# Optimization experiments

Hardware: AMD Instinct MI355X
Metric: run time of the kernel (lower is better)

Reference implementation:

```python
import jax, jax.numpy as jnp
import numpy as np

B, T, D = 2, 2048, 1024
H, G, K = 16, 4, 64          # num_heads, num_kv_heads, head_dim
R = H // G                   # GQA repeat factor
F = 4096                     # mlp_dim
EPS = 1e-6


def rms_norm(x, scale, eps=EPS):
    var = jnp.mean(x.astype(jnp.float32) ** 2, axis=-1, keepdims=True)
    normed = x * jax.lax.rsqrt(var + eps)
    return (scale * normed).astype(x.dtype)


def apply_rope(x_BTHK, sin_BTK, cos_BTK):
    half = x_BTHK.shape[-1] // 2
    x1, x2 = x_BTHK[..., :half], x_BTHK[..., half:]
    s = sin_BTK[:, :, None, :]
    c = cos_BTK[:, :, None, :]
    return jnp.concatenate([x1 * c - x2 * s, x2 * c + x1 * s], axis=-1).astype(x_BTHK.dtype)


def setup_inputs() -> dict:
    key = jax.random.key(0)
    ks = jax.random.split(key, 12)
    hidden_BTD = jax.random.normal(ks[0], (B, T, D), jnp.float32)
    # rope tables: realistic sin/cos of position*inv_freq
    inv_freq = 1.0 / (10000.0 ** (jnp.arange(K // 2, dtype=jnp.float32) / (K // 2)))
    ang = jnp.arange(T, dtype=jnp.float32)[:, None] * inv_freq[None, :]  # [T, K/2]
    sin_BTK = jnp.broadcast_to(jnp.sin(ang)[None], (B, T, K // 2))
    cos_BTK = jnp.broadcast_to(jnp.cos(ang)[None], (B, T, K // 2))
    mask = jnp.broadcast_to(jnp.tril(jnp.ones((T, T), bool))[None], (B, T, T))
    sc = 1.0 / np.sqrt(D)
    scf = 1.0 / np.sqrt(F)
    return {
        "hidden_BTD": hidden_BTD, "sin_BTK": sin_BTK, "cos_BTK": cos_BTK, "mask": mask,
        "ln1_scale": jnp.ones((D,), jnp.float32),
        "ln2_scale": jnp.ones((D,), jnp.float32),
        "qn_scale": jnp.ones((K,), jnp.float32),
        "kn_scale": jnp.ones((K,), jnp.float32),
        "q_w": jax.random.normal(ks[1], (D, H * K), jnp.float32) * sc,
        "k_w": jax.random.normal(ks[2], (D, G * K), jnp.float32) * sc,
        "v_w": jax.random.normal(ks[3], (D, G * K), jnp.float32) * sc,
        "o_w": jax.random.normal(ks[4], (H * K, D), jnp.float32) * sc,
        "gate_w": jax.random.normal(ks[5], (D, F), jnp.float32) * sc,
        "up_w": jax.random.normal(ks[6], (D, F), jnp.float32) * sc,
        "down_w": jax.random.normal(ks[7], (F, D), jnp.float32) * scf,
    }


def reference(hidden_BTD, sin_BTK, cos_BTK, mask, ln1_scale, ln2_scale,
              qn_scale, kn_scale, q_w, k_w, v_w, o_w, gate_w, up_w, down_w):
    x = rms_norm(hidden_BTD, ln1_scale)
    q = rms_norm((x @ q_w).reshape(B, T, H, K), qn_scale)
    k = rms_norm((x @ k_w).reshape(B, T, G, K), kn_scale)
    v = (x @ v_w).reshape(B, T, G, K)
    q = apply_rope(q, sin_BTK, cos_BTK)
    k = apply_rope(k, sin_BTK, cos_BTK)
    q_BTGRK = q.reshape(B, T, G, R, K)
    scale = K ** (-0.5)
    logits = jnp.einsum('BTGRK,BSGK->BTSGR', q_BTGRK, k) * scale
    neg = float(jnp.finfo(logits.dtype).min)
    logits = jnp.where(mask[:, :, :, None, None], logits, neg)
    weights = jax.nn.softmax(logits.astype(jnp.float32), axis=2).astype(logits.dtype)
    attn = jnp.einsum('BTSGR,BSGK->BTGRK', weights, v).reshape(B, T, H * K)
    hidden_BTD = hidden_BTD + attn @ o_w
    y = rms_norm(hidden_BTD, ln2_scale)
    ff = (jax.nn.silu(y @ gate_w) * (y @ up_w)) @ down_w
    return hidden_BTD + ff
```

## Files before the change

kernel.cpp:

```cpp
#include <hip/hip_runtime.h>
#include <hip/hip_bf16.h>

#define EPSF 1e-6f
constexpr int Bsz  = 2;
constexpr int Tseq = 2048;
constexpr int Dmod = 1024;
constexpr int Hh   = 16;
constexpr int Gg   = 4;
constexpr int Ff   = 4096;
constexpr int Mrows = Bsz * Tseq;

typedef __attribute__((ext_vector_type(8))) short bf16x8;
typedef __attribute__((ext_vector_type(4))) float f32x4;
typedef unsigned short u16;

__device__ inline u16 f2bf(float x) {
    union { float f; unsigned u; } v; v.f = x;
    unsigned r = v.u + 0x7fff + ((v.u >> 16) & 1);
    return (u16)(r >> 16);
}
__device__ inline float bf2f(u16 h) {
    union { unsigned u; float f; } v; v.u = ((unsigned)h) << 16; return v.f;
}

__device__ __forceinline__ void async_copy16(const u16* g, u16* l) {
    __builtin_amdgcn_global_load_lds(
        (const __attribute__((address_space(1))) void*)g,
        (__attribute__((address_space(3))) void*)l, 16, 0, 0);
}


__global__ __launch_bounds__(256) void wprep_all_kernel(
    const float* __restrict__ q_w, const float* __restrict__ k_w,
    const float* __restrict__ v_w, const float* __restrict__ o_w,
    const float* __restrict__ gate_w, const float* __restrict__ up_w,
    const float* __restrict__ down_w,
    u16* __restrict__ QKVT, u16* __restrict__ OTh, u16* __restrict__ OTl,
    u16* __restrict__ GTh, u16* __restrict__ UTh, u16* __restrict__ DTh)
{
    const int bx = blockIdx.x;
    const float* W; u16* Th; u16* Tl = nullptr;
    int N, Kd, ntile, ktile, drow;
    if (bx < 1024) {
        W = q_w; N = 1024; Kd = 1024; ntile = bx & 31; ktile = bx >> 5;
        Th = QKVT; drow = ntile * 32;
    } else if (bx < 1280) {
        const int i = bx - 1024;
        W = k_w; N = 256; Kd = 1024; ntile = i & 7; ktile = i >> 3;
        Th = QKVT; drow = 1024 + ntile * 32;
    } else if (bx < 1536) {
        const int i = bx - 1280;
        W = v_w; N = 256; Kd = 1024; ntile = i & 7; ktile = i >> 3;
        Th = QKVT; drow = 1280 + ntile * 32;
    } else if (bx < 2560) {
        const int i = bx - 1536;
        W = o_w; N = 1024; Kd = 1024; ntile = i & 31; ktile = i >> 5;
        Th = OTh; Tl = OTl; drow = ntile * 32;
    } else if (bx < 6656) {
        const int i = bx - 2560;
        W = gate_w; N = 4096; Kd = 1024; ntile = i & 127; ktile = i >> 7;
        Th = GTh; drow = ntile * 32;
    } else if (bx < 10752) {
        const int i = bx - 6656;
        W = up_w; N = 4096; Kd = 1024; ntile = i & 127; ktile = i >> 7;
        Th = UTh; drow = ntile * 32;
    } else {
        const int i = bx - 10752;
        W = down_w; N = 1024; Kd = 4096; ntile = i & 31; ktile = i >> 5;
        Th = DTh; drow = ntile * 32;
    }
    const int n0 = ntile * 32, k0 = ktile * 32;

    __shared__ float tile[32][33];
    const int r = threadIdx.x >> 3, c4 = (threadIdx.x & 7) * 4;
    const float4 v = *reinterpret_cast<const float4*>(&W[(size_t)(k0 + r) * N + n0 + c4]);
    tile[r][c4 + 0] = v.x; tile[r][c4 + 1] = v.y;
    tile[r][c4 + 2] = v.z; tile[r][c4 + 3] = v.w;
    __syncthreads();
    const int nl = threadIdx.x >> 3, kq = (threadIdx.x & 7) * 4;
    float x0 = tile[kq + 0][nl], x1 = tile[kq + 1][nl];
    float x2 = tile[kq + 2][nl], x3 = tile[kq + 3][nl];
    ushort4 h;
    h.x = f2bf(x0); h.y = f2bf(x1); h.z = f2bf(x2); h.w = f2bf(x3);
    *reinterpret_cast<ushort4*>(&Th[(size_t)(drow + nl) * Kd + k0 + kq]) = h;
    if (Tl) {
        ushort4 l;
        l.x = f2bf(x0 - bf2f(h.x)); l.y = f2bf(x1 - bf2f(h.y));
        l.z = f2bf(x2 - bf2f(h.z)); l.w = f2bf(x3 - bf2f(h.w));
        *reinterpret_cast<ushort4*>(&Tl[(size_t)(drow + nl) * Kd + k0 + kq]) = l;
    }
}

template <int LO>
__global__ __launch_bounds__(256) void rmsnorm_split_kernel(
    const float* __restrict__ x, const float* __restrict__ scale,
    u16* __restrict__ oh, u16* __restrict__ ol)
{
    const int row = blockIdx.x;
    const int tid = threadIdx.x;
    const float4 v = reinterpret_cast<const float4*>(x + (size_t)row * Dmod)[tid];
    float ss = v.x * v.x + v.y * v.y + v.z * v.z + v.w * v.w;
    #pragma unroll
    for (int off = 32; off; off >>= 1) ss += __shfl_xor(ss, off, 64);
    __shared__ float part[4];
    if ((tid & 63) == 0) part[tid >> 6] = ss;
    __syncthreads();
    const float tot = part[0] + part[1] + part[2] + part[3];
    const float rstd = rsqrtf(tot * (1.0f / Dmod) + EPSF);
    const float4 sc = reinterpret_cast<const float4*>(scale)[tid];
    float o0 = v.x * rstd * sc.x, o1 = v.y * rstd * sc.y;
    float o2 = v.z * rstd * sc.z, o3 = v.w * rstd * sc.w;
    ushort4 h;
    h.x = f2bf(o0); h.y = f2bf(o1); h.z = f2bf(o2); h.w = f2bf(o3);
    *reinterpret_cast<ushort4*>(&oh[(size_t)row * Dmod + tid * 4]) = h;
    if (LO) {
        ushort4 l;
        l.x = f2bf(o0 - bf2f(h.x)); l.y = f2bf(o1 - bf2f(h.y));
        l.z = f2bf(o2 - bf2f(h.z)); l.w = f2bf(o3 - bf2f(h.w));
        *reinterpret_cast<ushort4*>(&ol[(size_t)row * Dmod + tid * 4]) = l;
    }
}

template <int NKT, int ASPLIT, int BSPLIT, int RES>
__global__ __launch_bounds__(256, 2) void mfma_gemm_pipe(
    const u16* __restrict__ Ah, const u16* __restrict__ Al,
    const u16* __restrict__ Bh, const u16* __restrict__ Bl,
    const float* __restrict__ res, float* __restrict__ C,
    int M, int N)
{
    constexpr int Kd = NKT * 32;
    constexpr int NI = 4 + 2 * ASPLIT + 2 * BSPLIT;
    static_assert((NKT - 2) % 3 == 0, "main loop unroll-3");

    __shared__ u16 AsH[3][128 * 32];
    __shared__ u16 BsH[3][128 * 32];
    __shared__ u16 AsL[ASPLIT ? 3 : 1][128 * 32];
    __shared__ u16 BsL[BSPLIT ? 3 : 1][128 * 32];

    const int tid = threadIdx.x;
    const int lane = tid & 63, wave = tid >> 6;
    const int wm = (wave >> 1) * 64, wn = (wave & 1) * 64;
    const int m0 = blockIdx.y * 128, n0 = blockIdx.x * 128;
    const int fm = lane & 15, quad = lane >> 4;
    const int fsw = (fm >> 1) & 3;
    const int fcol = (quad ^ fsw) * 8;

    f32x4 acc[4][4];
    #pragma unroll
    for (int i = 0; i < 4; ++i)
        #pragma unroll
        for (int j = 0; j < 4; ++j) acc[i][j] = (f32x4){0.f, 0.f, 0.f, 0.f};

    const int srow = tid >> 2;
    const int schk = tid & 3;
    const int sw   = schk ^ ((srow >> 1) & 3);
    const u16* aS0 = &Ah[(size_t)(m0 + srow) * Kd + sw * 8];
    const u16* aS1 = &Ah[(size_t)(m0 + srow + 64) * Kd + sw * 8];
    const u16* bS0 = &Bh[(size_t)(n0 + srow) * Kd + sw * 8];
    const u16* bS1 = &Bh[(size_t)(n0 + srow + 64) * Kd + sw * 8];
    const u16* alS0 = ASPLIT ? &Al[(size_t)(m0 + srow) * Kd + sw * 8] : nullptr;
    const u16* alS1 = ASPLIT ? &Al[(size_t)(m0 + srow + 64) * Kd + sw * 8] : nullptr;
    const u16* blS0 = BSPLIT ? &Bl[(size_t)(n0 + srow) * Kd + sw * 8] : nullptr;
    const u16* blS1 = BSPLIT ? &Bl[(size_t)(n0 + srow + 64) * Kd + sw * 8] : nullptr;
    const int dst0 = srow * 32 + schk * 8;
    const int dst1 = dst0 + 64 * 32;

#define PSTAGE(T, BUF) do {                                                  \
        async_copy16(aS0 + (T) * 32, &AsH[BUF][dst0]);                       \
        async_copy16(aS1 + (T) * 32, &AsH[BUF][dst1]);                       \
        if (ASPLIT) {                                                        \
            async_copy16(alS0 + (T) * 32, &AsL[BUF][dst0]);                  \
            async_copy16(alS1 + (T) * 32, &AsL[BUF][dst1]);                  \
        }                                                                    \
        async_copy16(bS0 + (T) * 32, &BsH[BUF][dst0]);                       \
        async_copy16(bS1 + (T) * 32, &BsH[BUF][dst1]);                       \
        if (BSPLIT) {                                                        \
            async_copy16(blS0 + (T) * 32, &BsL[BUF][dst0]);                  \
            async_copy16(blS1 + (T) * 32, &BsL[BUF][dst1]);                  \
        }                                                                    \
    } while (0)

#define PGATE(GATE) do {                                                     \
        if ((GATE) == 1) {                                                   \
            if constexpr (NI == 4)                                           \
                asm volatile("s_waitcnt vmcnt(4)" ::: "memory");             \
            else                                                             \
                asm volatile("s_waitcnt vmcnt(8)" ::: "memory");             \
        } else if ((GATE) == 0) {                                            \
            asm volatile("s_waitcnt vmcnt(0)" ::: "memory");                 \
        }                                                                    \
    } while (0)

#define PSTEP(BC, BN, T, PF, GATE) do {                                      \
    bf16x8 ah[4], bh[4], al[4], bl[4];                                       \
    _Pragma("unroll")                                                        \
    for (int t = 0; t < 4; ++t) {                                            \
        const int ra = (wm + t * 16 + fm) * 32 + fcol;                       \
        const int rb = (wn + t * 16 + fm) * 32 + fcol;                       \
        ah[t] = *reinterpret_cast<const bf16x8*>(&AsH[BC][ra]);              \
        bh[t] = *reinterpret_cast<const bf16x8*>(&BsH[BC][rb]);              \
        if (ASPLIT) al[t] = *reinterpret_cast<const bf16x8*>(&AsL[BC][ra]);  \
        if (BSPLIT) bl[t] = *reinterpret_cast<const bf16x8*>(&BsL[BC][rb]);  \
    }                                                                        \
    if (PF) PSTAGE((T) + 2, BN);                                             \
    __builtin_amdgcn_s_barrier();                                            \
    asm volatile("s_waitcnt lgkmcnt(0)" ::: "memory");                       \
    __builtin_amdgcn_sched_barrier(0);                                       \
    __builtin_amdgcn_s_setprio(1);                                           \
    _Pragma("unroll")                                                        \
    for (int mt = 0; mt < 4; ++mt)                                           \
        _Pragma("unroll")                                                    \
        for (int nt = 0; nt < 4; ++nt) {                                     \
            acc[mt][nt] = __builtin_amdgcn_mfma_f32_16x16x32_bf16(           \
                ah[mt], bh[nt], acc[mt][nt], 0, 0, 0);                       \
            if (BSPLIT)                                                      \
                acc[mt][nt] = __builtin_amdgcn_mfma_f32_16x16x32_bf16(       \
                    ah[mt], bl[nt], acc[mt][nt], 0, 0, 0);                   \
            if (ASPLIT)                                                      \
                acc[mt][nt] = __builtin_amdgcn_mfma_f32_16x16x32_bf16(       \
                    al[mt], bh[nt], acc[mt][nt], 0, 0, 0);                   \
        }                                                                    \
    __builtin_amdgcn_s_setprio(0);                                           \
    PGATE(GATE);                                                             \
    __builtin_amdgcn_s_barrier();                                            \
} while (0)

    PSTAGE(0, 0);
    PSTAGE(1, 1);
    PGATE(1);
    __builtin_amdgcn_s_barrier();

    #pragma unroll 1
    for (int t3 = 0; t3 < NKT - 2; t3 += 3) {
        PSTEP(0, 2, t3 + 0, true, 1);
        PSTEP(1, 0, t3 + 1, true, 1);
        PSTEP(2, 1, t3 + 2, true, 1);
    }
    PSTEP(0, 2, NKT - 2, false, 0);
    PSTEP(1, 0, NKT - 1, false, -1);

#undef PSTEP
#undef PGATE
#undef PSTAGE

    const int cr = (lane >> 4) * 4, cn = lane & 15;
    #pragma unroll
    for (int mt = 0; mt < 4; ++mt)
        #pragma unroll
        for (int nt = 0; nt < 4; ++nt)
            #pragma unroll
            for (int r = 0; r < 4; ++r) {
                const int gm = m0 + wm + mt * 16 + cr + r;
                const int gn = n0 + wn + nt * 16 + cn;
                float v = acc[mt][nt][r];
                if (RES) v += res[(size_t)gm * N + gn];
                C[(size_t)gm * N + gn] = v;
            }
}

__global__ __launch_bounds__(256, 2) void qkv_fused_kernel(
    const u16* __restrict__ Ah, const u16* __restrict__ Bh,
    const float* __restrict__ qn, const float* __restrict__ kn,
    const float* __restrict__ sinp, const float* __restrict__ cosp,
    u16* __restrict__ Qbh, u16* __restrict__ Qbl,
    u16* __restrict__ Kbh, u16* __restrict__ Kbl,
    u16* __restrict__ Vth, u16* __restrict__ Vtl)
{
    constexpr int Kd = 1024;
    constexpr int NKT = 32;
    __shared__ u16 As[3][128 * 32];
    __shared__ u16 Bs[3][128 * 32];

    const int tid = threadIdx.x;
    const int lane = tid & 63, wave = tid >> 6;
    const int wm = (wave >> 1) * 64, wn = (wave & 1) * 64;
    const int m0 = blockIdx.y * 128, n0 = blockIdx.x * 128;
    const int fm = lane & 15, quad = lane >> 4;
    const int fsw = (fm >> 1) & 3;
    const int fcol = ((quad ^ fsw) * 8);

    f32x4 acc[4][4];
    #pragma unroll
    for (int i = 0; i < 4; ++i)
        #pragma unroll
        for (int j = 0; j < 4; ++j) acc[i][j] = (f32x4){0.f, 0.f, 0.f, 0.f};

    const int srow = tid >> 2;
    const int schk = tid & 3;
    const int sw   = schk ^ ((srow >> 1) & 3);
    const u16* aS0 = &Ah[(size_t)(m0 + srow) * Kd + sw * 8];
    const u16* aS1 = &Ah[(size_t)(m0 + srow + 64) * Kd + sw * 8];
    const u16* bS0 = &Bh[(size_t)(n0 + srow) * Kd + sw * 8];
    const u16* bS1 = &Bh[(size_t)(n0 + srow + 64) * Kd + sw * 8];
    const int dst0 = srow * 32 + schk * 8;
    const int dst1 = dst0 + 64 * 32;

#define QSTAGE(T, BUF) do {                                                  \
        async_copy16(aS0 + (T) * 32, &As[BUF][dst0]);                        \
        async_copy16(aS1 + (T) * 32, &As[BUF][dst1]);                        \
        async_copy16(bS0 + (T) * 32, &Bs[BUF][dst0]);                        \
        async_copy16(bS1 + (T) * 32, &Bs[BUF][dst1]);                        \
    } while (0)

#define QSTEP(BC, BN, T, PF, GATE) do {                                      \
    bf16x8 ah[4], bh[4];                                                     \
    _Pragma("unroll")                                                        \
    for (int t = 0; t < 4; ++t) {                                            \
        ah[t] = *reinterpret_cast<const bf16x8*>(                            \
            &As[BC][(wm + t * 16 + fm) * 32 + fcol]);                        \
        bh[t] = *reinterpret_cast<const bf16x8*>(                            \
            &Bs[BC][(wn + t * 16 + fm) * 32 + fcol]);                        \
    }                                                                        \
    if (PF) QSTAGE((T) + 2, BN);                                             \
    __builtin_amdgcn_s_barrier();                                            \
    asm volatile("s_waitcnt lgkmcnt(0)" ::: "memory");                       \
    __builtin_amdgcn_sched_barrier(0);                                       \
    __builtin_amdgcn_s_setprio(1);                                           \
    _Pragma("unroll")                                                        \
    for (int mt = 0; mt < 4; ++mt)                                           \
        _Pragma("unroll")                                                    \
        for (int nt = 0; nt < 4; ++nt)                                       \
            acc[mt][nt] = __builtin_amdgcn_mfma_f32_16x16x32_bf16(           \
                ah[mt], bh[nt], acc[mt][nt], 0, 0, 0);                       \
    __builtin_amdgcn_s_setprio(0);                                           \
    if ((GATE) == 1) {                                                       \
        asm volatile("s_waitcnt vmcnt(4)" ::: "memory");                     \
    } else if ((GATE) == 0) {                                                \
        asm volatile("s_waitcnt vmcnt(0)" ::: "memory");                     \
    }                                                                        \
    __builtin_amdgcn_s_barrier();                                            \
} while (0)

    QSTAGE(0, 0);
    QSTAGE(1, 1);
    asm volatile("s_waitcnt vmcnt(4)" ::: "memory");
    __builtin_amdgcn_s_barrier();

    #pragma unroll 1
    for (int t3 = 0; t3 < NKT - 2; t3 += 3) {
        QSTEP(0, 2, t3 + 0, true, 1);
        QSTEP(1, 0, t3 + 1, true, 1);
        QSTEP(2, 1, t3 + 2, true, 1);
    }
    QSTEP(0, 2, NKT - 2, false, 0);
    QSTEP(1, 0, NKT - 1, false, -1);

#undef QSTEP
#undef QSTAGE

    const int gn0 = n0 + wn;
    const int l15 = lane & 15;

    if (gn0 < 1280) {
        const bool isQ = (gn0 < 1024);
        const float* nsc = isQ ? qn : kn;
        const float osc = isQ ? 0.125f : 1.0f;
        u16* __restrict__ oh = isQ ? Qbh : Kbh;
        u16* __restrict__ ol = isQ ? Qbl : Kbl;
        const int rowstride = isQ ? 1024 : 256;
        const int colbase = isQ ? gn0 : gn0 - 1024;
        float sc[4];
        #pragma unroll
        for (int nt = 0; nt < 4; ++nt) sc[nt] = nsc[nt * 16 + l15];

        #pragma unroll
        for (int mt = 0; mt < 4; ++mt)
            #pragma unroll
            for (int r = 0; r < 4; ++r) {
                const int bt = m0 + wm + mt * 16 + quad * 4 + r;
                float v[4];
                #pragma unroll
                for (int nt = 0; nt < 4; ++nt) v[nt] = acc[mt][nt][r];
                float ss = v[0] * v[0] + v[1] * v[1] + v[2] * v[2] + v[3] * v[3];
                #pragma unroll
                for (int off = 1; off < 16; off <<= 1)
                    ss += __shfl_xor(ss, off, 16);
                const float rstd = rsqrtf(ss * (1.0f / 64.0f) + EPSF);
                float nv[4];
                #pragma unroll
                for (int nt = 0; nt < 4; ++nt) nv[nt] = v[nt] * rstd * sc[nt];
                const float s0 = sinp[bt * 32 + l15];
                const float c0 = cosp[bt * 32 + l15];
                const float s1 = sinp[bt * 32 + 16 + l15];
                const float c1 = cosp[bt * 32 + 16 + l15];
                float o[4];
                o[0] = (nv[0] * c0 - nv[2] * s0) * osc;
                o[1] = (nv[1] * c1 - nv[3] * s1) * osc;
                o[2] = (nv[2] * c0 + nv[0] * s0) * osc;
                o[3] = (nv[3] * c1 + nv[1] * s1) * osc;
                #pragma unroll
                for (int nt = 0; nt < 4; ++nt) {
                    const size_t off = (size_t)bt * rowstride + colbase + nt * 16 + l15;
                    const u16 hi = f2bf(o[nt]);
                    oh[off] = hi;
                    ol[off] = f2bf(o[nt] - bf2f(hi));
                }
            }
    } else {
        const int g = (gn0 - 1280) >> 6;
        const int b = (m0 + wm) >> 11;
        const int tb = ((m0 + wm) & 2047) + quad * 4;
        #pragma unroll
        for (int mt = 0; mt < 4; ++mt)
            #pragma unroll
            for (int nt = 0; nt < 4; ++nt) {
                const float v0 = acc[mt][nt][0], v1 = acc[mt][nt][1];
                const float v2 = acc[mt][nt][2], v3 = acc[mt][nt][3];
                ushort4 hv, lv;
                hv.x = f2bf(v0); hv.y = f2bf(v1); hv.z = f2bf(v2); hv.w = f2bf(v3);
                lv.x = f2bf(v0 - bf2f(hv.x)); lv.y = f2bf(v1 - bf2f(hv.y));
                lv.z = f2bf(v2 - bf2f(hv.z)); lv.w = f2bf(v3 - bf2f(hv.w));
                const size_t off =
                    ((size_t)((b * 4 + g) * 64 + nt * 16 + l15)) * Tseq + tb + mt * 16;
                *reinterpret_cast<ushort4*>(&Vth[off]) = hv;
                *reinterpret_cast<ushort4*>(&Vtl[off]) = lv;
            }
    }
}

#define GU_PHASE_SYNC()                                       \
    __builtin_amdgcn_s_barrier();                             \
    asm volatile("s_waitcnt lgkmcnt(0)" ::: "memory");        \
    __builtin_amdgcn_sched_barrier(0)

#define GU_MFMA16(AF, NB0)                                                       \
    _Pragma("unroll")                                                            \
    for (int mf = 0; mf < 4; ++mf) {                                             \
        accg[mf][(NB0)] = __builtin_amdgcn_mfma_f32_16x16x32_bf16(               \
            AF[mf], bgf[(NB0)], accg[mf][(NB0)], 0, 0, 0);                       \
        accu[mf][(NB0)] = __builtin_amdgcn_mfma_f32_16x16x32_bf16(               \
            AF[mf], buf2[(NB0)], accu[mf][(NB0)], 0, 0, 0);                      \
        accg[mf][(NB0) + 1] = __builtin_amdgcn_mfma_f32_16x16x32_bf16(           \
            AF[mf], bgf[(NB0) + 1], accg[mf][(NB0) + 1], 0, 0, 0);               \
        accu[mf][(NB0) + 1] = __builtin_amdgcn_mfma_f32_16x16x32_bf16(           \
            AF[mf], buf2[(NB0) + 1], accu[mf][(NB0) + 1], 0, 0, 0);              \
    }

__global__ __launch_bounds__(512, 2) void gateup8_kernel(
    const u16* __restrict__ Yh, const u16* __restrict__ Yl,
    const u16* __restrict__ Gw, const u16* __restrict__ Uw,
    u16* __restrict__ FF)
{
    constexpr int NK = 32;
    __shared__ u16 AsH[3][256 * 32];
    __shared__ u16 AsL[3][256 * 32];
    __shared__ u16 Gs[3][128 * 32];
    __shared__ u16 Us[3][128 * 32];

    const int tid  = threadIdx.x;
    const int lane = tid & 63;
    const int wave = tid >> 6;
    const int wave_m = wave >> 1;
    const int wave_n = wave & 1;

    const int wg  = blockIdx.x;
    const int xcd = wg & 7;
    const int idx = wg >> 3;
    const int ntile = xcd * 4 + (idx & 3);
    const int mtile = idx >> 2;
    const int m0 = mtile * 256, n0 = ntile * 128;

    const int fm = lane & 15, quad = lane >> 4;
    const int fsw = (fm >> 1) & 3;
    const int fcol = (quad ^ fsw) * 8;

    f32x4 accg[4][4], accu[4][4];
    #pragma unroll
    for (int i = 0; i < 4; ++i)
        #pragma unroll
        for (int j = 0; j < 4; ++j) {
            accg[i][j] = (f32x4){0.f, 0.f, 0.f, 0.f};
            accu[i][j] = (f32x4){0.f, 0.f, 0.f, 0.f};
        }

    const int srow = tid >> 2;
    const int schk = tid & 3;
    const int sw   = schk ^ ((srow >> 1) & 3);
    const u16* aSrc0 = &Yh[(size_t)(m0 + srow) * 1024 + sw * 8];
    const u16* aSrc1 = &Yh[(size_t)(m0 + srow + 128) * 1024 + sw * 8];
    const u16* lSrc0 = &Yl[(size_t)(m0 + srow) * 1024 + sw * 8];
    const u16* lSrc1 = &Yl[(size_t)(m0 + srow + 128) * 1024 + sw * 8];
    const u16* gSrc  = &Gw[(size_t)(n0 + srow) * 1024 + sw * 8];
    const u16* uSrc  = &Uw[(size_t)(n0 + srow) * 1024 + sw * 8];
    const int aDst0 = srow * 32 + schk * 8;
    const int aDst1 = aDst0 + 128 * 32;

#define STAGE_AH(T, BUF) do {                                  \
        async_copy16(aSrc0 + (T) * 32, &AsH[BUF][aDst0]);      \
        async_copy16(aSrc1 + (T) * 32, &AsH[BUF][aDst1]); } while (0)
#define STAGE_AL(T, BUF) do {                                  \
        async_copy16(lSrc0 + (T) * 32, &AsL[BUF][aDst0]);      \
        async_copy16(lSrc1 + (T) * 32, &AsL[BUF][aDst1]); } while (0)
#define STAGE_B(T, BUF) do {                                   \
        async_copy16(gSrc + (T) * 32, &Gs[BUF][aDst0]);        \
        async_copy16(uSrc + (T) * 32, &Us[BUF][aDst0]); } while (0)

    int raOff[4], rbOff[4];
    #pragma unroll
    for (int mf = 0; mf < 4; ++mf)
        raOff[mf] = (wave_m * 64 + mf * 16 + fm) * 32 + fcol;
    #pragma unroll
    for (int nf = 0; nf < 4; ++nf)
        rbOff[nf] = (wave_n * 64 + nf * 16 + fm) * 32 + fcol;

    STAGE_AH(0, 0); STAGE_AL(0, 0); STAGE_B(0, 0);
    STAGE_AH(1, 1); STAGE_AL(1, 1); STAGE_B(1, 1);
    asm volatile("s_waitcnt vmcnt(6)" ::: "memory");
    __builtin_amdgcn_s_barrier();

    int bcur = 0, bnxt = 2;
    #pragma unroll 1
    for (int t = 0; t < NK; ++t) {
        const bool pf = (t + 2 < NK);
        bf16x8 bgf[4], buf2[4];
        bf16x8 ahf[4];

        {
            #pragma unroll
            for (int nf = 0; nf < 4; ++nf) {
                bgf[nf]  = *reinterpret_cast<const bf16x8*>(&Gs[bcur][rbOff[nf]]);
                buf2[nf] = *reinterpret_cast<const bf16x8*>(&Us[bcur][rbOff[nf]]);
            }
            #pragma unroll
            for (int mf = 0; mf < 4; ++mf)
                ahf[mf] = *reinterpret_cast<const bf16x8*>(&AsH[bcur][raOff[mf]]);
            if (pf) STAGE_AH(t + 2, bnxt);
            GU_PHASE_SYNC();
            __builtin_amdgcn_s_setprio(1);
            GU_MFMA16(ahf, 0);
            __builtin_amdgcn_s_setprio(0);
            __builtin_amdgcn_s_barrier();
        }
        {
            if (pf) STAGE_AL(t + 2, bnxt);
            GU_PHASE_SYNC();
            __builtin_amdgcn_s_setprio(1);
            GU_MFMA16(ahf, 2);
            __builtin_amdgcn_s_setprio(0);
            __builtin_amdgcn_s_barrier();
        }
        bf16x8 alf[4];
        {
            #pragma unroll
            for (int mf = 0; mf < 4; ++mf)
                alf[mf] = *reinterpret_cast<const bf16x8*>(&AsL[bcur][raOff[mf]]);
            if (pf) STAGE_B(t + 2, bnxt);
            GU_PHASE_SYNC();
            __builtin_amdgcn_s_setprio(1);
            GU_MFMA16(alf, 0);
            __builtin_amdgcn_s_setprio(0);
            __builtin_amdgcn_s_barrier();
        }
        {
            GU_PHASE_SYNC();
            __builtin_amdgcn_s_setprio(1);
            GU_MFMA16(alf, 2);
            __builtin_amdgcn_s_setprio(0);
            if (t + 2 < NK) {
                asm volatile("s_waitcnt vmcnt(6)" ::: "memory");
            } else if (t + 1 < NK) {
                asm volatile("s_waitcnt vmcnt(0)" ::: "memory");
            }
            __builtin_amdgcn_s_barrier();
        }

        bcur = (bcur == 2) ? 0 : bcur + 1;
        bnxt = (bnxt == 2) ? 0 : bnxt + 1;
    }
#undef STAGE_AH
#undef STAGE_AL
#undef STAGE_B

    const int cr = quad * 4;
    #pragma unroll
    for (int mf = 0; mf < 4; ++mf)
        #pragma unroll
        for (int nf = 0; nf < 4; ++nf)
            #pragma unroll
            for (int r = 0; r < 4; ++r) {
                const int gm = m0 + wave_m * 64 + mf * 16 + cr + r;
                const int gn = n0 + wave_n * 64 + nf * 16 + fm;
                const float g = accg[mf][nf][r];
                const float ff = (g / (1.0f + __expf(-g))) * accu[mf][nf][r];
                FF[(size_t)gm * Ff + gn] = f2bf(ff);
            }
}

__global__ __launch_bounds__(256) void attn_mfma_kernel(
    const u16* __restrict__ Qh, const u16* __restrict__ Ql,
    const u16* __restrict__ Kh, const u16* __restrict__ Kl,
    const u16* __restrict__ Vth, const u16* __restrict__ Vtl,
    u16* __restrict__ AOh, u16* __restrict__ AOl)
{
    __shared__ u16 KsH[64 * 72];
    __shared__ u16 KsL[64 * 72];
    __shared__ u16 VsH[64 * 72];
    __shared__ u16 VsL[64 * 72];
    __shared__ u16 Ps[4][16 * 72];

    const int tid = threadIdx.x;
    const int wave = tid >> 6, lane = tid & 63;
    const int l15 = lane & 15, quad = lane >> 4;

    const int bg = blockIdx.x & 7;
    const int b = bg >> 2, g = bg & 3;
    const int win = 127 - (blockIdx.x >> 3);
    const int t0 = win * 16;
    const int h = g * 4 + wave;

    bf16x8 qh[2], ql[2];
    {
        const size_t qrow = (size_t)(b * Tseq + t0 + l15) * 1024 + h * 64;
        #pragma unroll
        for (int ks = 0; ks < 2; ++ks) {
            qh[ks] = *reinterpret_cast<const bf16x8*>(&Qh[qrow + ks * 32 + quad * 8]);
            ql[ks] = *reinterpret_cast<const bf16x8*>(&Ql[qrow + ks * 32 + quad * 8]);
        }
    }

    const int srow = tid >> 2;
    const int scol = (tid & 3) * 16;
    const size_t kgb = (size_t)(b * Tseq) * 256 + g * 64 + scol;
    const size_t vgb = (size_t)(bg * 64 + srow) * Tseq + scol;

    const int nit = t0 / 64 + 1;

    uint4 ck0, ck1, cl0, cl1, cv0, cv1, cw0, cw1;
    {
        const size_t ka = kgb + (size_t)srow * 256;
        ck0 = *reinterpret_cast<const uint4*>(&Kh[ka]);
        ck1 = *reinterpret_cast<const uint4*>(&Kh[ka + 8]);
        cl0 = *reinterpret_cast<const uint4*>(&Kl[ka]);
        cl1 = *reinterpret_cast<const uint4*>(&Kl[ka + 8]);
        cv0 = *reinterpret_cast<const uint4*>(&Vth[vgb]);
        cv1 = *reinterpret_cast<const uint4*>(&Vth[vgb + 8]);
        cw0 = *reinterpret_cast<const uint4*>(&Vtl[vgb]);
        cw1 = *reinterpret_cast<const uint4*>(&Vtl[vgb + 8]);
    }

    f32x4 oacc[4];
    #pragma unroll
    for (int nt = 0; nt < 4; ++nt) oacc[nt] = (f32x4){0.f, 0.f, 0.f, 0.f};
    float m_r[4], l_r[4];
    #pragma unroll
    for (int r = 0; r < 4; ++r) { m_r[r] = -1e30f; l_r[r] = 0.0f; }

    u16* psw = &Ps[wave][0];
    const int lb = srow * 72 + scol;

    for (int it = 0; it < nit; ++it) {
        const int s0 = it * 64;
        const bool diag = (it == nit - 1);

        __syncthreads();
        *reinterpret_cast<uint4*>(&KsH[lb])     = ck0;
        *reinterpret_cast<uint4*>(&KsH[lb + 8]) = ck1;
        *reinterpret_cast<uint4*>(&KsL[lb])     = cl0;
        *reinterpret_cast<uint4*>(&KsL[lb + 8]) = cl1;
        *reinterpret_cast<uint4*>(&VsH[lb])     = cv0;
        *reinterpret_cast<uint4*>(&VsH[lb + 8]) = cv1;
        *reinterpret_cast<uint4*>(&VsL[lb])     = cw0;
        *reinterpret_cast<uint4*>(&VsL[lb + 8]) = cw1;
        if (it + 1 < nit) {
            const size_t ka = kgb + (size_t)(s0 + 64 + srow) * 256;
            ck0 = *reinterpret_cast<const uint4*>(&Kh[ka]);
            ck1 = *reinterpret_cast<const uint4*>(&Kh[ka + 8]);
            cl0 = *reinterpret_cast<const uint4*>(&Kl[ka]);
            cl1 = *reinterpret_cast<const uint4*>(&Kl[ka + 8]);
            const size_t va = vgb + s0 + 64;
            cv0 = *reinterpret_cast<const uint4*>(&Vth[va]);
            cv1 = *reinterpret_cast<const uint4*>(&Vth[va + 8]);
            cw0 = *reinterpret_cast<const uint4*>(&Vtl[va]);
            cw1 = *reinterpret_cast<const uint4*>(&Vtl[va + 8]);
        }
        __syncthreads();

        f32x4 sacc[4];
        #pragma unroll
        for (int nt = 0; nt < 4; ++nt) sacc[nt] = (f32x4){0.f, 0.f, 0.f, 0.f};

        #pragma unroll
        for (int ks = 0; ks < 2; ++ks) {
            bf16x8 kfh[4], kfl[4];
            #pragma unroll
            for (int nt = 0; nt < 4; ++nt) {
                const int a = (nt * 16 + l15) * 72 + ks * 32 + quad * 8;
                kfh[nt] = *reinterpret_cast<const bf16x8*>(&KsH[a]);
                kfl[nt] = *reinterpret_cast<const bf16x8*>(&KsL[a]);
            }
            #pragma unroll
            for (int nt = 0; nt < 4; ++nt) {
                sacc[nt] = __builtin_amdgcn_mfma_f32_16x16x32_bf16(qh[ks], kfh[nt], sacc[nt], 0, 0, 0);
                sacc[nt] = __builtin_amdgcn_mfma_f32_16x16x32_bf16(ql[ks], kfh[nt], sacc[nt], 0, 0, 0);
                sacc[nt] = __builtin_amdgcn_mfma_f32_16x16x32_bf16(qh[ks], kfl[nt], sacc[nt], 0, 0, 0);
            }
        }

        if (diag) {
            #pragma unroll
            for (int nt = 0; nt < 4; ++nt) {
                const int sg = s0 + nt * 16 + l15;
                #pragma unroll
                for (int r = 0; r < 4; ++r)
                    if (sg > t0 + quad * 4 + r) sacc[nt][r] = -1e30f;
            }
        }

        #pragma unroll
        for (int r = 0; r < 4; ++r) {
            float mx = fmaxf(fmaxf(sacc[0][r], sacc[1][r]),
                             fmaxf(sacc[2][r], sacc[3][r]));
            #pragma unroll
            for (int off = 1; off < 16; off <<= 1)
                mx = fmaxf(mx, __shfl_xor(mx, off, 16));
            const float mnew = fmaxf(m_r[r], mx);
            const float alpha = __expf(m_r[r] - mnew);
            m_r[r] = mnew;

            float rs = 0.0f;
            #pragma unroll
            for (int nt = 0; nt < 4; ++nt) {
                const float p = __expf(sacc[nt][r] - mnew);
                sacc[nt][r] = p;
                rs += p;
            }
            #pragma unroll
            for (int off = 1; off < 16; off <<= 1)
                rs += __shfl_xor(rs, off, 16);
            l_r[r] = l_r[r] * alpha + rs;
            #pragma unroll
            for (int nt = 0; nt < 4; ++nt) oacc[nt][r] *= alpha;
            #pragma unroll
            for (int nt = 0; nt < 4; ++nt)
                psw[(quad * 4 + r) * 72 + nt * 16 + l15] = f2bf(sacc[nt][r]);
        }

        #pragma unroll
        for (int ks = 0; ks < 2; ++ks) {
            const bf16x8 pa = *reinterpret_cast<const bf16x8*>(
                &psw[l15 * 72 + ks * 32 + quad * 8]);
            bf16x8 vfh[4], vfl[4];
            #pragma unroll
            for (int nt = 0; nt < 4; ++nt) {
                const int a = (nt * 16 + l15) * 72 + ks * 32 + quad * 8;
                vfh[nt] = *reinterpret_cast<const bf16x8*>(&VsH[a]);
                vfl[nt] = *reinterpret_cast<const bf16x8*>(&VsL[a]);
            }
            #pragma unroll
            for (int nt = 0; nt < 4; ++nt) {
                oacc[nt] = __builtin_amdgcn_mfma_f32_16x16x32_bf16(pa, vfh[nt], oacc[nt], 0, 0, 0);
                oacc[nt] = __builtin_amdgcn_mfma_f32_16x16x32_bf16(pa, vfl[nt], oacc[nt], 0, 0, 0);
            }
        }
    }

    #pragma unroll
    for (int r = 0; r < 4; ++r) {
        const float inv = 1.0f / l_r[r];
        const size_t orow = (size_t)(b * Tseq + t0 + quad * 4 + r) * 1024 + h * 64;
        #pragma unroll
        for (int nt = 0; nt < 4; ++nt) {
            const float o = oacc[nt][r] * inv;
            const u16 hi = f2bf(o);
            AOh[orow + nt * 16 + l15] = hi;
            AOl[orow + nt * 16 + l15] = f2bf(o - bf2f(hi));
        }
    }
}

extern "C" void kernel_launch(void* const* d_in, const int* in_sizes, int n_in,
                              void* d_out, int out_size, void* d_ws,
                              size_t ws_size, hipStream_t stream)
{
    const float* hidden = (const float*)d_in[0];
    const float* sinp   = (const float*)d_in[1];
    const float* cosp   = (const float*)d_in[2];
    const float* ln1    = (const float*)d_in[4];
    const float* ln2    = (const float*)d_in[5];
    const float* qn     = (const float*)d_in[6];
    const float* kn     = (const float*)d_in[7];
    const float* q_w    = (const float*)d_in[8];
    const float* k_w    = (const float*)d_in[9];
    const float* v_w    = (const float*)d_in[10];
    const float* o_w    = (const float*)d_in[11];
    const float* gate_w = (const float*)d_in[12];
    const float* up_w   = (const float*)d_in[13];
    const float* down_w = (const float*)d_in[14];
    float* out = (float*)d_out;

    char* base = (char*)d_ws;
    u16*   OTh  = (u16*)(base);
    u16*   OTl  = (u16*)(base + 2097152);
    u16*   GTh  = (u16*)(base + 4194304);
    u16*   UTh  = (u16*)(base + 12582912);
    u16*   DTh  = (u16*)(base + 20971520);
    u16*   QKVT = (u16*)(base + 29360128);
    u16*   Xh   = (u16*)(base + 32505856);
    u16*   Qbh  = (u16*)(base + 40894464);
    u16*   Qbl  = (u16*)(base + 49283072);
    u16*   Kbh  = (u16*)(base + 57671680);
    u16*   Kbl  = (u16*)(base + 59768832);
    u16*   Vth  = (u16*)(base + 61865984);
    u16*   Vtl  = (u16*)(base + 63963136);
    u16*   AOh  = (u16*)(base + 66060288);
    u16*   AOl  = (u16*)(base + 74448896);
    u16*   FFh  = (u16*)(base + 82837504);

    float* H2 = (float*)Qbh;
    u16*   Yh = Kbh;
    u16*   Yl = AOh;

    wprep_all_kernel<<<14848, 256, 0, stream>>>(
        q_w, k_w, v_w, o_w, gate_w, up_w, down_w,
        QKVT, OTh, OTl, GTh, UTh, DTh);

    rmsnorm_split_kernel<0><<<Mrows, 256, 0, stream>>>(hidden, ln1, Xh, nullptr);

    qkv_fused_kernel<<<dim3(12, 32), 256, 0, stream>>>(
        Xh, QKVT, qn, kn, sinp, cosp, Qbh, Qbl, Kbh, Kbl, Vth, Vtl);

    attn_mfma_kernel<<<Bsz * Gg * (Tseq / 16), 256, 0, stream>>>(
        Qbh, Qbl, Kbh, Kbl, Vth, Vtl, AOh, AOl);

    mfma_gemm_pipe<32, 1, 1, 1><<<dim3(8, 32), 256, 0, stream>>>(
        AOh, AOl, OTh, OTl, hidden, H2, Mrows, Dmod);

    rmsnorm_split_kernel<1><<<Mrows, 256, 0, stream>>>(H2, ln2, Yh, Yl);

    gateup8_kernel<<<512, 512, 0, stream>>>(Yh, Yl, GTh, UTh, FFh);

    mfma_gemm_pipe<128, 0, 0, 1><<<dim3(8, 32), 256, 0, stream>>>(
        FFh, nullptr, DTh, nullptr, H2, out, Mrows, Dmod);
}
```

Baseline: 496.2 us.

## Narrow output GEMM tiles to 128x64 and reshape gate/up wave layout to 2x4

The o-projection and down-projection GEMMs become templated on the N tile width and launch with BN=64. That doubles the grid from 256 to 512 blocks, so the CUs are better filled on a device with many compute units, at the cost of more A re-reads and a lower MFMA-to-load ratio. The gate/up kernel changes its 8 waves from a 4x2 to a 2x4 arrangement, with each wave covering 128x32 instead of 64x64. A fragments are now reloaded per half-phase, which changes LDS traffic and register pressure. Wait-count gating is adjusted to match the new number of loads per stage.

```diff
diff --git a/kernel.cpp b/kernel.cpp
--- a/kernel.cpp
+++ b/kernel.cpp
@@ -121,7 +121,7 @@
     }
 }
 
-template <int NKT, int ASPLIT, int BSPLIT, int RES>
+template <int NKT, int BN, int ASPLIT, int BSPLIT, int RES>
 __global__ __launch_bounds__(256, 2) void mfma_gemm_pipe(
     const u16* __restrict__ Ah, const u16* __restrict__ Al,
     const u16* __restrict__ Bh, const u16* __restrict__ Bl,
@@ -129,27 +129,28 @@
     int M, int N)
 {
     constexpr int Kd = NKT * 32;
-    constexpr int NI = 4 + 2 * ASPLIT + 2 * BSPLIT;
+    constexpr int NT = (BN / 2) / 16;
+    constexpr int NI = 2 + 2 * ASPLIT + (BN / 64) + (BN / 64) * BSPLIT;
     static_assert((NKT - 2) % 3 == 0, "main loop unroll-3");
 
     __shared__ u16 AsH[3][128 * 32];
-    __shared__ u16 BsH[3][128 * 32];
+    __shared__ u16 BsH[3][BN * 32];
     __shared__ u16 AsL[ASPLIT ? 3 : 1][128 * 32];
-    __shared__ u16 BsL[BSPLIT ? 3 : 1][128 * 32];
+    __shared__ u16 BsL[BSPLIT ? 3 : 1][BN * 32];
 
     const int tid = threadIdx.x;
     const int lane = tid & 63, wave = tid >> 6;
-    const int wm = (wave >> 1) * 64, wn = (wave & 1) * 64;
-    const int m0 = blockIdx.y * 128, n0 = blockIdx.x * 128;
+    const int wm = (wave >> 1) * 64, wn = (wave & 1) * (BN / 2);
+    const int m0 = blockIdx.y * 128, n0 = blockIdx.x * BN;
     const int fm = lane & 15, quad = lane >> 4;
     const int fsw = (fm >> 1) & 3;
     const int fcol = (quad ^ fsw) * 8;
 
-    f32x4 acc[4][4];
+    f32x4 acc[4][NT];
     #pragma unroll
     for (int i = 0; i < 4; ++i)
         #pragma unroll
-        for (int j = 0; j < 4; ++j) acc[i][j] = (f32x4){0.f, 0.f, 0.f, 0.f};
+        for (int j = 0; j < NT; ++j) acc[i][j] = (f32x4){0.f, 0.f, 0.f, 0.f};
 
     const int srow = tid >> 2;
     const int schk = tid & 3;
@@ -157,11 +158,11 @@
     const u16* aS0 = &Ah[(size_t)(m0 + srow) * Kd + sw * 8];
     const u16* aS1 = &Ah[(size_t)(m0 + srow + 64) * Kd + sw * 8];
     const u16* bS0 = &Bh[(size_t)(n0 + srow) * Kd + sw * 8];
-    const u16* bS1 = &Bh[(size_t)(n0 + srow + 64) * Kd + sw * 8];
+    const u16* bS1 = (BN == 128) ? &Bh[(size_t)(n0 + srow + 64) * Kd + sw * 8] : nullptr;
     const u16* alS0 = ASPLIT ? &Al[(size_t)(m0 + srow) * Kd + sw * 8] : nullptr;
     const u16* alS1 = ASPLIT ? &Al[(size_t)(m0 + srow + 64) * Kd + sw * 8] : nullptr;
     const u16* blS0 = BSPLIT ? &Bl[(size_t)(n0 + srow) * Kd + sw * 8] : nullptr;
-    const u16* blS1 = BSPLIT ? &Bl[(size_t)(n0 + srow + 64) * Kd + sw * 8] : nullptr;
+    const u16* blS1 = (BSPLIT && BN == 128) ? &Bl[(size_t)(n0 + srow + 64) * Kd + sw * 8] : nullptr;
     const int dst0 = srow * 32 + schk * 8;
     const int dst1 = dst0 + 64 * 32;
 
@@ -173,17 +174,21 @@
             async_copy16(alS1 + (T) * 32, &AsL[BUF][dst1]);                  \
         }                                                                    \
         async_copy16(bS0 + (T) * 32, &BsH[BUF][dst0]);                       \
-        async_copy16(bS1 + (T) * 32, &BsH[BUF][dst1]);                       \
+        if (BN == 128) async_copy16(bS1 + (T) * 32, &BsH[BUF][dst1]);        \
         if (BSPLIT) {                                                        \
             async_copy16(blS0 + (T) * 32, &BsL[BUF][dst0]);                  \
-            async_copy16(blS1 + (T) * 32, &BsL[BUF][dst1]);                  \
+            if (BN == 128) async_copy16(blS1 + (T) * 32, &BsL[BUF][dst1]);   \
         }                                                                    \
     } while (0)
 
 #define PGATE(GATE) do {                                                     \
         if ((GATE) == 1) {                                                   \
-            if constexpr (NI == 4)                                           \
+            if constexpr (NI == 3)                                           \
+                asm volatile("s_waitcnt vmcnt(3)" ::: "memory");             \
+            else if constexpr (NI == 4)                                      \
                 asm volatile("s_waitcnt vmcnt(4)" ::: "memory");             \
+            else if constexpr (NI == 6)                                      \
+                asm volatile("s_waitcnt vmcnt(6)" ::: "memory");             \
             else                                                             \
                 asm volatile("s_waitcnt vmcnt(8)" ::: "memory");             \
         } else if ((GATE) == 0) {                                            \
@@ -191,18 +196,21 @@
         }                                                                    \
     } while (0)
 
-#define PSTEP(BC, BN, T, PF, GATE) do {                                      \
-    bf16x8 ah[4], bh[4], al[4], bl[4];                                       \
+#define PSTEP(BC, BN_, T, PF, GATE) do {                                     \
+    bf16x8 ah[4], bh[NT], al[4], bl[NT];                                     \
     _Pragma("unroll")                                                        \
     for (int t = 0; t < 4; ++t) {                                            \
         const int ra = (wm + t * 16 + fm) * 32 + fcol;                       \
+        ah[t] = *reinterpret_cast<const bf16x8*>(&AsH[BC][ra]);              \
+        if (ASPLIT) al[t] = *reinterpret_cast<const bf16x8*>(&AsL[BC][ra]);  \
+    }                                                                        \
+    _Pragma("unroll")                                                        \
+    for (int t = 0; t < NT; ++t) {                                           \
         const int rb = (wn + t * 16 + fm) * 32 + fcol;                       \
-        ah[t] = *reinterpret_cast<const bf16x8*>(&AsH[BC][ra]);              \
         bh[t] = *reinterpret_cast<const bf16x8*>(&BsH[BC][rb]);              \
-        if (ASPLIT) al[t] = *reinterpret_cast<const bf16x8*>(&AsL[BC][ra]);  \
         if (BSPLIT) bl[t] = *reinterpret_cast<const bf16x8*>(&BsL[BC][rb]);  \
     }                                                                        \
-    if (PF) PSTAGE((T) + 2, BN);                                             \
+    if (PF) PSTAGE((T) + 2, BN_);                                            \
     __builtin_amdgcn_s_barrier();                                            \
     asm volatile("s_waitcnt lgkmcnt(0)" ::: "memory");                       \
     __builtin_amdgcn_sched_barrier(0);                                       \
@@ -210,7 +218,7 @@
     _Pragma("unroll")                                                        \
     for (int mt = 0; mt < 4; ++mt)                                           \
         _Pragma("unroll")                                                    \
-        for (int nt = 0; nt < 4; ++nt) {                                     \
+        for (int nt = 0; nt < NT; ++nt) {                                    \
             acc[mt][nt] = __builtin_amdgcn_mfma_f32_16x16x32_bf16(           \
                 ah[mt], bh[nt], acc[mt][nt], 0, 0, 0);                       \
             if (BSPLIT)                                                      \
@@ -247,7 +255,7 @@
     #pragma unroll
     for (int mt = 0; mt < 4; ++mt)
         #pragma unroll
-        for (int nt = 0; nt < 4; ++nt)
+        for (int nt = 0; nt < NT; ++nt)
             #pragma unroll
             for (int r = 0; r < 4; ++r) {
                 const int gm = m0 + wm + mt * 16 + cr + r;
@@ -423,17 +431,17 @@
     asm volatile("s_waitcnt lgkmcnt(0)" ::: "memory");        \
     __builtin_amdgcn_sched_barrier(0)
 
-#define GU_MFMA16(AF, NB0)                                                       \
+#define GU_MFMA4(MBASE, AF)                                                      \
     _Pragma("unroll")                                                            \
     for (int mf = 0; mf < 4; ++mf) {                                             \
-        accg[mf][(NB0)] = __builtin_amdgcn_mfma_f32_16x16x32_bf16(               \
-            AF[mf], bgf[(NB0)], accg[mf][(NB0)], 0, 0, 0);                       \
-        accu[mf][(NB0)] = __builtin_amdgcn_mfma_f32_16x16x32_bf16(               \
-            AF[mf], buf2[(NB0)], accu[mf][(NB0)], 0, 0, 0);                      \
-        accg[mf][(NB0) + 1] = __builtin_amdgcn_mfma_f32_16x16x32_bf16(           \
-            AF[mf], bgf[(NB0) + 1], accg[mf][(NB0) + 1], 0, 0, 0);               \
-        accu[mf][(NB0) + 1] = __builtin_amdgcn_mfma_f32_16x16x32_bf16(           \
-            AF[mf], buf2[(NB0) + 1], accu[mf][(NB0) + 1], 0, 0, 0);              \
+        accg[(MBASE) + mf][0] = __builtin_amdgcn_mfma_f32_16x16x32_bf16(         \
+            AF[mf], bgf[0], accg[(MBASE) + mf][0], 0, 0, 0);                     \
+        accu[(MBASE) + mf][0] = __builtin_amdgcn_mfma_f32_16x16x32_bf16(         \
+            AF[mf], buf2[0], accu[(MBASE) + mf][0], 0, 0, 0);                    \
+        accg[(MBASE) + mf][1] = __builtin_amdgcn_mfma_f32_16x16x32_bf16(         \
+            AF[mf], bgf[1], accg[(MBASE) + mf][1], 0, 0, 0);                     \
+        accu[(MBASE) + mf][1] = __builtin_amdgcn_mfma_f32_16x16x32_bf16(         \
+            AF[mf], buf2[1], accu[(MBASE) + mf][1], 0, 0, 0);                    \
     }
 
 __global__ __launch_bounds__(512, 2) void gateup8_kernel(
@@ -450,8 +458,8 @@
     const int tid  = threadIdx.x;
     const int lane = tid & 63;
     const int wave = tid >> 6;
-    const int wave_m = wave >> 1;
-    const int wave_n = wave & 1;
+    const int wave_m = wave >> 2;
+    const int wave_n = wave & 3;
 
     const int wg  = blockIdx.x;
     const int xcd = wg & 7;
@@ -464,11 +472,11 @@
     const int fsw = (fm >> 1) & 3;
     const int fcol = (quad ^ fsw) * 8;
 
-    f32x4 accg[4][4], accu[4][4];
-    #pragma unroll
-    for (int i = 0; i < 4; ++i)
-        #pragma unroll
-        for (int j = 0; j < 4; ++j) {
+    f32x4 accg[8][2], accu[8][2];
+    #pragma unroll
+    for (int i = 0; i < 8; ++i)
+        #pragma unroll
+        for (int j = 0; j < 2; ++j) {
             accg[i][j] = (f32x4){0.f, 0.f, 0.f, 0.f};
             accu[i][j] = (f32x4){0.f, 0.f, 0.f, 0.f};
         }
@@ -495,13 +503,13 @@
         async_copy16(gSrc + (T) * 32, &Gs[BUF][aDst0]);        \
         async_copy16(uSrc + (T) * 32, &Us[BUF][aDst0]); } while (0)
 
-    int raOff[4], rbOff[4];
-    #pragma unroll
-    for (int mf = 0; mf < 4; ++mf)
-        raOff[mf] = (wave_m * 64 + mf * 16 + fm) * 32 + fcol;
-    #pragma unroll
-    for (int nf = 0; nf < 4; ++nf)
-        rbOff[nf] = (wave_n * 64 + nf * 16 + fm) * 32 + fcol;
+    int raOff[8], rbOff[2];
+    #pragma unroll
+    for (int mf = 0; mf < 8; ++mf)
+        raOff[mf] = (wave_m * 128 + mf * 16 + fm) * 32 + fcol;
+    #pragma unroll
+    for (int nf = 0; nf < 2; ++nf)
+        rbOff[nf] = (wave_n * 32 + nf * 16 + fm) * 32 + fcol;
 
     STAGE_AH(0, 0); STAGE_AL(0, 0); STAGE_B(0, 0);
     STAGE_AH(1, 1); STAGE_AL(1, 1); STAGE_B(1, 1);
@@ -512,49 +520,57 @@
     #pragma unroll 1
     for (int t = 0; t < NK; ++t) {
         const bool pf = (t + 2 < NK);
-        bf16x8 bgf[4], buf2[4];
-        bf16x8 ahf[4];
+        bf16x8 bgf[2], buf2[2];
 
         {
             #pragma unroll
-            for (int nf = 0; nf < 4; ++nf) {
+            for (int nf = 0; nf < 2; ++nf) {
                 bgf[nf]  = *reinterpret_cast<const bf16x8*>(&Gs[bcur][rbOff[nf]]);
                 buf2[nf] = *reinterpret_cast<const bf16x8*>(&Us[bcur][rbOff[nf]]);
             }
+            bf16x8 af[4];
             #pragma unroll
             for (int mf = 0; mf < 4; ++mf)
-                ahf[mf] = *reinterpret_cast<const bf16x8*>(&AsH[bcur][raOff[mf]]);
+                af[mf] = *reinterpret_cast<const bf16x8*>(&AsH[bcur][raOff[mf]]);
             if (pf) STAGE_AH(t + 2, bnxt);
             GU_PHASE_SYNC();
             __builtin_amdgcn_s_setprio(1);
-            GU_MFMA16(ahf, 0);
+            GU_MFMA4(0, af);
             __builtin_amdgcn_s_setprio(0);
             __builtin_amdgcn_s_barrier();
         }
         {
+            bf16x8 af[4];
+            #pragma unroll
+            for (int mf = 0; mf < 4; ++mf)
+                af[mf] = *reinterpret_cast<const bf16x8*>(&AsH[bcur][raOff[mf + 4]]);
             if (pf) STAGE_AL(t + 2, bnxt);
             GU_PHASE_SYNC();
             __builtin_amdgcn_s_setprio(1);
-            GU_MFMA16(ahf, 2);
+            GU_MFMA4(4, af);
             __builtin_amdgcn_s_setprio(0);
             __builtin_amdgcn_s_barrier();
         }
-        bf16x8 alf[4];
         {
+            bf16x8 af[4];
             #pragma unroll
             for (int mf = 0; mf < 4; ++mf)
-                alf[mf] = *reinterpret_cast<const bf16x8*>(&AsL[bcur][raOff[mf]]);
+                af[mf] = *reinterpret_cast<const bf16x8*>(&AsL[bcur][raOff[mf]]);
             if (pf) STAGE_B(t + 2, bnxt);
             GU_PHASE_SYNC();
             __builtin_amdgcn_s_setprio(1);
-            GU_MFMA16(alf, 0);
+            GU_MFMA4(0, af);
             __builtin_amdgcn_s_setprio(0);
             __builtin_amdgcn_s_barrier();
         }
         {
+            bf16x8 af[4];
+            #pragma unroll
+            for (int mf = 0; mf < 4; ++mf)
+                af[mf] = *reinterpret_cast<const bf16x8*>(&AsL[bcur][raOff[mf + 4]]);
             GU_PHASE_SYNC();
             __builtin_amdgcn_s_setprio(1);
-            GU_MFMA16(alf, 2);
+            GU_MFMA4(4, af);
             __builtin_amdgcn_s_setprio(0);
             if (t + 2 < NK) {
                 asm volatile("s_waitcnt vmcnt(6)" ::: "memory");
@@ -573,13 +589,13 @@
 
     const int cr = quad * 4;
     #pragma unroll
-    for (int mf = 0; mf < 4; ++mf)
-        #pragma unroll
-        for (int nf = 0; nf < 4; ++nf)
+    for (int mf = 0; mf < 8; ++mf)
+        #pragma unroll
+        for (int nf = 0; nf < 2; ++nf)
             #pragma unroll
             for (int r = 0; r < 4; ++r) {
-                const int gm = m0 + wave_m * 64 + mf * 16 + cr + r;
-                const int gn = n0 + wave_n * 64 + nf * 16 + fm;
+                const int gm = m0 + wave_m * 128 + mf * 16 + cr + r;
+                const int gn = n0 + wave_n * 32 + nf * 16 + fm;
                 const float g = accg[mf][nf][r];
                 const float ff = (g / (1.0f + __expf(-g))) * accu[mf][nf][r];
                 FF[(size_t)gm * Ff + gn] = f2bf(ff);
@@ -822,13 +838,13 @@
     attn_mfma_kernel<<<Bsz * Gg * (Tseq / 16), 256, 0, stream>>>(
         Qbh, Qbl, Kbh, Kbl, Vth, Vtl, AOh, AOl);
 
-    mfma_gemm_pipe<32, 1, 1, 1><<<dim3(8, 32), 256, 0, stream>>>(
+    mfma_gemm_pipe<32, 64, 1, 1, 1><<<dim3(16, 32), 256, 0, stream>>>(
         AOh, AOl, OTh, OTl, hidden, H2, Mrows, Dmod);
 
     rmsnorm_split_kernel<1><<<Mrows, 256, 0, stream>>>(H2, ln2, Yh, Yl);
 
     gateup8_kernel<<<512, 512, 0, stream>>>(Yh, Yl, GTh, UTh, FFh);
 
-    mfma_gemm_pipe<128, 0, 0, 1><<<dim3(8, 32), 256, 0, stream>>>(
+    mfma_gemm_pipe<128, 64, 0, 0, 1><<<dim3(16, 32), 256, 0, stream>>>(
         FFh, nullptr, DTh, nullptr, H2, out, Mrows, Dmod);
 }
```

After: 496.8 us. Within noise of the previous version (+0.1%).
